# Kernel tuning notes

Hardware: AMD Instinct MI355X
Metric: run time of the kernel (lower is better)

Reference implementation:

```python
import jax, jax.numpy as jnp
import numpy as np

EPS = 1e-15


def _trace(t):
    return jnp.einsum('bii->b', t)


def _ortho_loss(ss, k):
    n = jnp.linalg.norm(ss, axis=(-1, -2), keepdims=True)
    diff = ss / n - jnp.eye(k, dtype=ss.dtype) / np.float32(np.sqrt(k))
    return jnp.mean(jnp.linalg.norm(diff, axis=(-1, -2)))


def _mincut_terms(s, adj):
    out_adj = jnp.einsum('bnk,bnm,bml->bkl', s, adj, s)
    d_flat = adj.sum(-1)  # degrees [B,N]
    num = _trace(out_adj)
    den = _trace(jnp.einsum('bnk,bn,bnl->bkl', s, d_flat, s)) + EPS
    return out_adj, num, den, d_flat


def dense_mincut_rewiring(x, adj, s, mask):
    k = s.shape[-1]  # 2
    m = mask[..., None].astype(x.dtype)
    s = jax.nn.softmax(s, axis=-1) * m
    _, num, den, _ = _mincut_terms(s, adj)
    mincut_loss = -jnp.mean(num / den)
    ortho_loss = _ortho_loss(jnp.einsum('bnk,bnl->bkl', s, s), k)
    # laplacian derivative of spectral gap wrt A_uv: (f_u - f_v)^2, f = soft bipartition
    f = s[..., 0]
    dlam = (f[:, :, None] - f[:, None, :]) ** 2
    return adj * (1.0 - dlam), mincut_loss, ortho_loss


def dense_CT_rewiring(x, adj, s, mask):
    k = s.shape[-1]
    m = mask[..., None].astype(x.dtype)
    s = jax.nn.softmax(s, axis=-1) * m
    d_flat = adj.sum(-1)
    sds = _trace(jnp.einsum('bnk,bn,bnl->bkl', s, d_flat, s))
    sas = _trace(jnp.einsum('bnk,bnm,bml->bkl', s, adj, s))
    den = _trace(jnp.einsum('bnk,bnl->bkl', s, s)) + EPS
    ct_loss = jnp.mean((sds - sas) / den)  # tr(Z^T L Z) / tr(Z^T Z)
    ortho_loss = _ortho_loss(jnp.einsum('bnk,bnl->bkl', s, s), k)
    # pairwise CT distances ||z_u - z_v|| / vol(G), sparsified by A
    sq = (s * s).sum(-1)
    d2 = sq[:, :, None] + sq[:, None, :] - 2.0 * jnp.einsum('bnk,bmk->bnm', s, s)
    ct_dist = jnp.sqrt(jnp.maximum(d2, 0.0) + 1e-12)
    vol = d_flat.sum(-1)
    new_adj = (ct_dist / (vol[:, None, None] + EPS)) * adj
    return new_adj, ct_loss, ortho_loss


def dense_mincut_pool(x, adj, s, mask):
    k = s.shape[-1]
    m = mask[..., None].astype(x.dtype)
    s = jax.nn.softmax(s, axis=-1) * m
    x = x * m
    out = jnp.einsum('bnk,bnf->bkf', s, x)
    out_adj, num, den, _ = _mincut_terms(s, adj)
    mincut_loss = -jnp.mean(num / den)
    ortho_loss = _ortho_loss(jnp.einsum('bnk,bnl->bkl', s, s), k)
    out_adj = out_adj * (1.0 - jnp.eye(k, dtype=adj.dtype))  # zero diagonal
    d = jnp.sqrt(out_adj.sum(-1)) + EPS  # [B,k]
    out_adj = out_adj / d[:, None, :] / d[:, :, None]
    return out, out_adj, mincut_loss, ortho_loss


def _dgc(x, adj, w_rel, b_rel, w_root):
    # DenseGraphConv(aggr='add'): lin_rel(A @ x) + lin_root(x)
    return jnp.matmul(adj, x) @ w_rel + b_rel + x @ w_root


def setup_inputs() -> dict:
    B, N, IN, H, KC, OUT, KMC = 16, 1024, 128, 32, 32, 10, 16
    keys = iter(jax.random.split(jax.random.key(0), 48))

    def lin(fin, fout):
        lim = float(1.0 / np.sqrt(fin))
        return (jax.random.uniform(next(keys), (fin, fout), jnp.float32, -lim, lim),
                jax.random.uniform(next(keys), (fout,), jnp.float32, -lim, lim))

    x = jax.random.normal(next(keys), (B, N, IN), jnp.float32)
    u = jax.random.uniform(next(keys), (B, N, N), jnp.float32)
    a = (u < 0.0156).astype(jnp.float32)  # avg degree ~16
    adj = jnp.maximum(a, jnp.swapaxes(a, 1, 2)) * (1.0 - jnp.eye(N, dtype=jnp.float32))
    mask = jnp.ones((B, N), dtype=bool)
    W1, b1 = lin(IN, H)
    Wrw, brw = lin(H, 2)
    Wg_rel, bg = lin(H, H); Wg_root, _ = lin(H, H)
    Wmcg, bmcg = lin(H, KMC)
    W2g_rel, b2g = lin(H, H); W2g_root, _ = lin(H, H)
    Wct, bct = lin(H, KC)
    Wc_rel, bc = lin(H, H); Wc_root, _ = lin(H, H)
    Wmcc, bmcc = lin(H, KMC)
    Wcat, bcat = lin(2 * H, H)
    W2, b2 = lin(H, H)
    W3, b3 = lin(H, OUT)
    return dict(x=x, adj=adj, mask=mask, W1=W1, b1=b1, Wrw=Wrw, brw=brw,
                Wg_rel=Wg_rel, bg=bg, Wg_root=Wg_root, Wmcg=Wmcg, bmcg=bmcg,
                W2g_rel=W2g_rel, b2g=b2g, W2g_root=W2g_root, Wct=Wct, bct=bct,
                Wc_rel=Wc_rel, bc=bc, Wc_root=Wc_root, Wmcc=Wmcc, bmcc=bmcc,
                Wcat=Wcat, bcat=bcat, W2=W2, b2=b2, W3=W3, b3=b3)


def reference(x, adj, mask, W1, b1, Wrw, brw, Wg_rel, bg, Wg_root, Wmcg, bmcg,
              W2g_rel, b2g, W2g_root, Wct, bct, Wc_rel, bc, Wc_root, Wmcc, bmcc,
              Wcat, bcat, W2, b2, W3, b3):
    x = x @ W1 + b1
    # GAP branch
    adj_gap, mc_rw, ol_rw = dense_mincut_rewiring(x, adj, x @ Wrw + brw, mask)
    x_gap = _dgc(x, adj_gap, Wg_rel, bg, Wg_root)
    x_gap, adj_gap, mc1, ol1 = dense_mincut_pool(x_gap, adj_gap, x_gap @ Wmcg + bmcg, mask)
    x_gap = _dgc(x_gap, adj_gap, W2g_rel, b2g, W2g_root)
    # CT branch
    adj_ct, ct_loss, ol_ct = dense_CT_rewiring(x, adj, x @ Wct + bct, mask)
    x_ct = _dgc(x, adj_ct, Wc_rel, bc, Wc_root)
    x_ct, adj_ct, mc2, ol2 = dense_mincut_pool(x_ct, adj_ct, x_ct @ Wmcc + bmcc, mask)
    x_ct = _dgc(x_ct, adj_ct, W2g_rel, b2g, W2g_root)  # source reuses self.conv2gap here
    h = jax.nn.relu(jnp.concatenate([x_gap, x_ct], axis=2) @ Wcat + bcat).sum(axis=1)
    h = jax.nn.relu(h @ W2 + b2)
    logits = h @ W3 + b3
    main_loss = mc_rw + ct_loss + mc1 + mc2
    ortho_loss = ol_rw + ol_ct + ol1 + ol2
    return (jax.nn.log_softmax(logits, axis=-1), main_loss, ortho_loss)
```

## Files before the change

### kernel.cpp

```cpp
#include <hip/hip_runtime.h>
#include <math.h>

#define BB   16
#define NNODE 1024
#define INF_ 128
#define HH   32
#define KMC  16
#define CAP  128
#define EPS15 1e-15f

typedef float v4f __attribute__((ext_vector_type(4)));

#define OFF_X      0
#define OFF_SRW    524288
#define OFF_SQCT   557056
#define OFF_SCT    573440
#define OFF_D      1097728
#define OFF_NUMRW  1114112
#define OFF_SAS    1130496
#define OFF_DGAP   1146880
#define OFF_DCT    1163264
#define OFF_XGAP   2228224
#define OFF_XCT    2752512
#define OFF_S2G    3276800
#define OFF_S2C    3538944
#define OFF_FROB   4325376
#define OFF_VOL    4325888
#define OFF_OUTG   4326032
#define OFF_OUTC   4334224
#define OFF_G2G    4342416
#define OFF_G2C    4346512
#define OFF_OAG    4350608
#define OFF_OAC    4354704
#define OFF_ENNZ   4358800
#define OFF_EIDX   4375184
#define OFF_EWG    5423760
#define OFF_EWC    7520912
#define OFF_PACK   9618064
#define OFF_BSUM   9683600

__device__ __forceinline__ float wave_sum(float v) {
#pragma unroll
  for (int off = 32; off >= 1; off >>= 1) v += __shfl_xor(v, off, 64);
  return v;
}

__device__ __forceinline__ void wave_sum4(float& a, float& b, float& c, float& d) {
#pragma unroll
  for (int off = 32; off >= 1; off >>= 1) {
    a += __shfl_xor(a, off, 64);
    b += __shfl_xor(b, off, 64);
    c += __shfl_xor(c, off, 64);
    d += __shfl_xor(d, off, 64);
  }
}

__device__ __forceinline__ float blk_sum(float v, float* sred, int tid) {
  v = wave_sum(v);
  __syncthreads();
  if ((tid & 63) == 0) sred[tid >> 6] = v;
  __syncthreads();
  return sred[0] + sred[1] + sred[2] + sred[3];
}

__device__ __forceinline__ void blk_sum5(float* v, float (*sm)[4], int tid) {
  int w = tid >> 6, lane = tid & 63;
#pragma unroll
  for (int i = 0; i < 5; i++) {
#pragma unroll
    for (int off = 32; off >= 1; off >>= 1) v[i] += __shfl_xor(v[i], off, 64);
  }
  if (lane == 0) {
#pragma unroll
    for (int i = 0; i < 5; i++) sm[i][w] = v[i];
  }
  __syncthreads();
#pragma unroll
  for (int i = 0; i < 5; i++) v[i] = sm[i][0] + sm[i][1] + sm[i][2] + sm[i][3];
}

__global__ __launch_bounds__(256) void k_fused0(
    const float* __restrict__ adj, const float* __restrict__ x,
    const float* __restrict__ W1, const float* __restrict__ b1,
    const float* __restrict__ Wrw, const float* __restrict__ brw,
    const float* __restrict__ Wct, const float* __restrict__ bct,
    float* __restrict__ ws)
{
  __shared__ __align__(16) float sW1[INF_*HH];
  __shared__ __align__(16) float sWct[HH*HH];
  __shared__ float sWrw[HH*2];
  __shared__ float sb1[HH], sbct[HH], sbrw[2];
  __shared__ __align__(16) float sx[8*INF_];
  __shared__ float sX[8*HH];
  __shared__ unsigned int s_e32[4][4][CAP/2];
  int tid = threadIdx.x;
  if (blockIdx.x < 1024) {
    int w = tid >> 6, lane = tid & 63;
    int row0 = blockIdx.x * 16 + w * 4;
    v4f v[16];
#pragma unroll
    for (int rr = 0; rr < 4; rr++) {
      const v4f* ar = (const v4f*)(adj + (size_t)(row0 + rr) * NNODE);
#pragma unroll
      for (int it = 0; it < 4; it++)
        v[rr*4 + it] = __builtin_nontemporal_load(&ar[it*64 + lane]);
    }
#pragma unroll
    for (int rr = 0; rr < 4; rr++) {
      int row = row0 + rr;
      int c = 0;
#pragma unroll
      for (int it = 0; it < 4; it++) {
        v4f a4 = v[rr*4 + it];
        c += (a4.x != 0.f) + (a4.y != 0.f) + (a4.z != 0.f) + (a4.w != 0.f);
      }
      int p = c;
#pragma unroll
      for (int off = 1; off < 64; off <<= 1) {
        int t = __shfl_up(p, off, 64);
        if (lane >= off) p += t;
      }
      int excl = p - c;
      int total = __shfl(p, 63, 64);
      unsigned short* es = (unsigned short*)s_e32[w][rr];
      int pos = excl;
#pragma unroll
      for (int it = 0; it < 4; it++) {
        v4f a4 = v[rr*4 + it];
        int m0 = it*256 + lane*4;
        if (a4.x != 0.f) { if (pos < CAP) es[pos] = (unsigned short)(m0+0); pos++; }
        if (a4.y != 0.f) { if (pos < CAP) es[pos] = (unsigned short)(m0+1); pos++; }
        if (a4.z != 0.f) { if (pos < CAP) es[pos] = (unsigned short)(m0+2); pos++; }
        if (a4.w != 0.f) { if (pos < CAP) es[pos] = (unsigned short)(m0+3); pos++; }
      }
      int nnzc = total < CAP ? total : CAP;
      unsigned int* dst = (unsigned int*)((unsigned short*)(ws + OFF_EIDX) + (size_t)row*CAP);
      int n32 = (nnzc + 1) >> 1;
      if (lane < n32) dst[lane] = s_e32[w][rr][lane];
      if (lane == 0) {
        ((int*)(ws + OFF_ENNZ))[row] = nnzc;
        ws[OFF_D + row] = (float)total;
      }
    }
  } else {
    for (int i = tid; i < INF_*HH/4; i += 256)
      ((float4*)sW1)[i] = ((const float4*)W1)[i];
    ((float4*)sWct)[tid] = ((const float4*)Wct)[tid];
    if (tid < HH*2) sWrw[tid] = Wrw[tid];
    if (tid < HH) { sb1[tid] = b1[tid]; sbct[tid] = bct[tid]; }
    if (tid < 2) sbrw[tid] = brw[tid];
    size_t row0 = (size_t)(blockIdx.x - 1024) * 8;
    ((float4*)sx)[tid] = ((const float4*)(x + row0 * INF_))[tid];
    __syncthreads();
    int r = tid >> 5, h = tid & 31;
    float acc = sb1[h];
#pragma unroll 8
    for (int k = 0; k < INF_; k++) acc += sx[r*INF_ + k] * sW1[k*HH + h];
    size_t row = row0 + r;
    ws[OFF_X + row*HH + h] = acc;
    sX[r*HH + h] = acc;
    __syncthreads();
    float sraw = sbct[h];
#pragma unroll
    for (int k = 0; k < HH; k++) sraw += sX[r*HH + k] * sWct[k*HH + h];
    float mx = sraw;
#pragma unroll
    for (int off = 16; off >= 1; off >>= 1) mx = fmaxf(mx, __shfl_xor(mx, off, 32));
    float e = __expf(sraw - mx);
    float sum = e;
#pragma unroll
    for (int off = 16; off >= 1; off >>= 1) sum += __shfl_xor(sum, off, 32);
    float sv = e / sum;
    ws[OFF_SCT + row*HH + h] = sv;
    float sq = sv * sv;
#pragma unroll
    for (int off = 16; off >= 1; off >>= 1) sq += __shfl_xor(sq, off, 32);
    float xv = sX[r*HH + h];
    float t0 = xv * sWrw[h*2 + 0];
    float t1 = xv * sWrw[h*2 + 1];
#pragma unroll
    for (int off = 16; off >= 1; off >>= 1) { t0 += __shfl_xor(t0, off, 32); t1 += __shfl_xor(t1, off, 32); }
    if (h == 0) {
      ws[OFF_SQCT + row] = sq;
      float r0 = t0 + sbrw[0], r1 = t1 + sbrw[1];
      float m2 = fmaxf(r0, r1);
      float e0 = __expf(r0 - m2), e1 = __expf(r1 - m2);
      float inv = 1.0f / (e0 + e1);
      float s0 = e0*inv, s1 = e1*inv;
      ((float2*)(ws + OFF_SRW))[row] = make_float2(s0, s1);
      ((float4*)(ws + OFF_PACK))[row] = make_float4(s0, s1, sq, 0.f);
    }
  }
}

__global__ __launch_bounds__(256) void k_edgefeat(
    const float* __restrict__ Wg_rel, const float* __restrict__ bg, const float* __restrict__ Wg_root,
    const float* __restrict__ Wc_rel, const float* __restrict__ bc, const float* __restrict__ Wc_root,
    const float* __restrict__ Wmcg, const float* __restrict__ bmcg,
    const float* __restrict__ Wmcc, const float* __restrict__ bmcc,
    float* __restrict__ out, float* __restrict__ ws)
{
  __shared__ unsigned short s_m[4][CAP];
  __shared__ float s_wg[4][CAP];
  __shared__ float s_wc[4][CAP];
  __shared__ float sp[8][32];
  __shared__ float sred[4];
  __shared__ __align__(16) float sWgrel[HH*HH], sWgroot[HH*HH], sWcrel[HH*HH], sWcroot[HH*HH];
  __shared__ float sbg[HH], sbc[HH];
  __shared__ float sYg[4*HH], sYc[4*HH], sXr[4*HH], sxg[4*HH], sxc[4*HH];
  int tid = threadIdx.x;
  if (blockIdx.x < 4096) {
    int xcd = blockIdx.x & 7;
    int idx = blockIdx.x >> 3;
    int b = xcd*2 + (idx >> 8);
    int chunk = idx & 255;
    int base4 = b*NNODE + chunk*4;
    ((float4*)sWgrel)[tid]  = ((const float4*)Wg_rel)[tid];
    ((float4*)sWgroot)[tid] = ((const float4*)Wg_root)[tid];
    ((float4*)sWcrel)[tid]  = ((const float4*)Wc_rel)[tid];
    ((float4*)sWcroot)[tid] = ((const float4*)Wc_root)[tid];
    if (tid < HH)  { sbg[tid] = bg[tid]; sbc[tid] = bc[tid]; }
    if (tid < 128) sXr[tid] = ws[OFF_X + (size_t)base4*HH + tid];
    float vp = 0.f;
#pragma unroll
    for (int i = 0; i < 4; i++) vp += ws[OFF_D + (size_t)b*NNODE + tid + i*256];

    const float* X = ws + OFF_X;
    const float2* srw = (const float2*)(ws + OFF_SRW);
    const float* sqct = ws + OFF_SQCT;
    const float* sct = ws + OFF_SCT;
    const float4* pack = (const float4*)(ws + OFF_PACK) + (size_t)b*NNODE;
    int w = tid >> 6, lane = tid & 63;
    int tm = lane & 3;
    int row = base4 + w;
    int nnz = ((const int*)(ws + OFF_ENNZ))[row];
    const unsigned short* eidx = (const unsigned short*)(ws + OFF_EIDX) + (size_t)row*CAP;
    const float4* cn4 = (const float4*)(sct + (size_t)row * HH);
    float4 c0 = cn4[tm*2], c1 = cn4[tm*2 + 1];
    float2 srwn = srw[row];
    float f_n = srwn.x;
    float sq_n = sqct[row];
    float numrw_p = 0.f, sas_p = 0.f, dg_p = 0.f, dc_p = 0.f;
    for (int e = (lane >> 2); e < nnz; e += 16) {
      int m = eidx[e];
      const float4* cm4 = (const float4*)(sct + ((size_t)b*NNODE + m) * HH);
      float4 d0 = cm4[tm*2], d1 = cm4[tm*2 + 1];
      float dot = c0.x*d0.x + c0.y*d0.y + c0.z*d0.z + c0.w*d0.w
                + c1.x*d1.x + c1.y*d1.y + c1.z*d1.z + c1.w*d1.w;
      dot += __shfl_xor(dot, 1, 64);
      dot += __shfl_xor(dot, 2, 64);
      float4 pk = pack[m];
      numrw_p += srwn.x*pk.x + srwn.y*pk.y;
      float df = f_n - pk.x;
      float wg = 1.0f - df*df;
      float d2 = sq_n + pk.z - 2.0f*dot;
      float wc = sqrtf(fmaxf(d2, 0.0f) + 1e-12f);
      sas_p += dot;
      dg_p += wg;
      dc_p += wc;
      if (tm == 0) {
        s_m[w][e] = (unsigned short)m;
        s_wg[w][e] = wg;
        s_wc[w][e] = wc;
        size_t eo = (size_t)row*CAP + e;
        ws[OFF_EWG + eo] = wg;
        ws[OFF_EWC + eo] = wc;
      }
    }
    wave_sum4(numrw_p, sas_p, dg_p, dc_p);
    if (lane == 0) {
      ws[OFF_NUMRW + row] = numrw_p * 0.25f;
      ws[OFF_SAS + row] = sas_p * 0.25f;
      ws[OFF_DGAP + row] = dg_p * 0.25f;
      ws[OFF_DCT + row] = dc_p * 0.25f;
    }
    int eoff = lane >> 4, hp = lane & 15;
    float yg0 = 0.f, yg1 = 0.f, yc0 = 0.f, yc1 = 0.f;
    for (int e = eoff; e < nnz; e += 4) {
      int m = s_m[w][e];
      float wg = s_wg[w][e], wc = s_wc[w][e];
      float2 xv = ((const float2*)(X + ((size_t)b*NNODE + m)*HH))[hp];
      yg0 += wg*xv.x; yg1 += wg*xv.y;
      yc0 += wc*xv.x; yc1 += wc*xv.y;
    }
    yg0 += __shfl_xor(yg0, 16, 64); yg0 += __shfl_xor(yg0, 32, 64);
    yg1 += __shfl_xor(yg1, 16, 64); yg1 += __shfl_xor(yg1, 32, 64);
    yc0 += __shfl_xor(yc0, 16, 64); yc0 += __shfl_xor(yc0, 32, 64);
    yc1 += __shfl_xor(yc1, 16, 64); yc1 += __shfl_xor(yc1, 32, 64);
    if (eoff == 0) {
      sYg[w*HH + 2*hp] = yg0; sYg[w*HH + 2*hp + 1] = yg1;
      sYc[w*HH + 2*hp] = yc0; sYc[w*HH + 2*hp + 1] = yc1;
    }
    float vol = blk_sum(vp, sred, tid);
    float ivol = 1.0f / (vol + EPS15);
    {
      int r = tid >> 6;
      int h = (tid >> 1) & 31;
      int half = tid & 1;
      int kb = half * 16;
      float accg = 0.f, accg2 = 0.f, accc = 0.f, accc2 = 0.f;
#pragma unroll
      for (int kk = 0; kk < 16; kk++) {
        int k = kb + kk;
        float ygv = sYg[r*HH + k], Xv = sXr[r*HH + k], ycv = sYc[r*HH + k];
        accg  += ygv * sWgrel[k*HH + h];
        accg2 += Xv  * sWgroot[k*HH + h];
        accc  += ycv * sWcrel[k*HH + h];
        accc2 += Xv  * sWcroot[k*HH + h];
      }
      accg  += __shfl_xor(accg, 1, 64);
      accg2 += __shfl_xor(accg2, 1, 64);
      accc  += __shfl_xor(accc, 1, 64);
      accc2 += __shfl_xor(accc2, 1, 64);
      if (half == 0) {
        float xgv = sbg[h] + accg + accg2;
        float xcv = sbc[h] + ivol*accc + accc2;
        size_t rw = (size_t)base4 + r;
        ws[OFF_XGAP + rw*HH + h] = xgv;
        ws[OFF_XCT  + rw*HH + h] = xcv;
        sxg[r*HH + h] = xgv;
        sxc[r*HH + h] = xcv;
      }
    }
    __syncthreads();
    if (tid < 128) {
      int r = tid >> 5, h = tid & 31;
      int j = h & 15, halfsel = h >> 4;
      const float* sin_ = halfsel ? sxc : sxg;
      const float* sw = halfsel ? Wmcc : Wmcg;
      float raw = halfsel ? bmcc[j] : bmcg[j];
#pragma unroll
      for (int k = 0; k < HH; k++) raw += sin_[r*HH + k] * sw[k*KMC + j];
      float mx = raw;
#pragma unroll
      for (int off = 8; off >= 1; off >>= 1) mx = fmaxf(mx, __shfl_xor(mx, off, 16));
      float e = __expf(raw - mx);
      float sum = e;
#pragma unroll
      for (int off = 8; off >= 1; off >>= 1) sum += __shfl_xor(sum, off, 16);
      float sv = e / sum;
      size_t rw = (size_t)base4 + r;
      if (halfsel == 0) ws[OFF_S2G + rw*KMC + j] = sv;
      else              ws[OFF_S2C + rw*KMC + j] = sv;
    }
  } else if (blockIdx.x < 4608) {
    int blk = blockIdx.x - 4096;
    int xcd = blk & 7;
    int idx = blk >> 3;
    int b = xcd*2 + (idx >> 5);
    int i = idx & 31;
    const float* sct = ws + OFF_SCT + (size_t)b*NNODE*HH;
    int j = tid & 31, seg = tid >> 5;
    float acc = 0.f;
    for (int n = seg*128; n < seg*128 + 128; n++)
      acc += sct[n*HH + i] * sct[n*HH + j];
    sp[seg][j] = acc;
    __syncthreads();
    if (tid < 32) {
      float g = 0.f;
#pragma unroll
      for (int s = 0; s < 8; s++) g += sp[s][tid];
      float p = g * g;
#pragma unroll
      for (int off = 16; off >= 1; off >>= 1) p += __shfl_xor(p, off, 32);
      if (tid == 0) ws[OFF_FROB + b*32 + i] = p;
    }
  } else {
    int b = blockIdx.x - 4608;
    if (b == 0 && tid < 2) out[160 + tid] = 0.f;
    if (tid < 12) ws[OFF_BSUM + b*12 + tid] = 0.f;
    for (int i = tid; i < 2048; i += 256) ws[OFF_OUTG + b*2048 + i] = 0.f;
    float vp = 0.f;
    for (int n = tid; n < NNODE; n += 256) vp += ws[OFF_D + (size_t)b*NNODE + n];
    float vol = blk_sum(vp, sred, tid);
    if (tid == 0) ws[OFF_VOL + b] = vol;
  }
}

__global__ __launch_bounds__(512) void k_passred(float* __restrict__ ws)
{
  __shared__ float sg[32*16], sc[32*16], stg[32*16], stc[32*16];
  __shared__ float sxg[32*32], sxc[32*32];
  int xcd = blockIdx.x & 7;
  int idx = blockIdx.x >> 3;
  int b = xcd*2 + (idx >> 5);
  int chunk = idx & 31;
  int tid = threadIdx.x;
  size_t n0 = (size_t)b * NNODE + chunk * 32;
  const float* pG  = ws + OFF_S2G  + n0 * KMC;
  const float* pC  = ws + OFF_S2C  + n0 * KMC;
  const float* pXG = ws + OFF_XGAP + n0 * HH;
  const float* pXC = ws + OFF_XCT  + n0 * HH;
  sg[tid] = pG[tid];
  sc[tid] = pC[tid];
  sxg[tid] = pXG[tid]; sxg[tid + 512] = pXG[tid + 512];
  sxc[tid] = pXC[tid]; sxc[tid + 512] = pXC[tid + 512];
  {
    int r = tid >> 4, k = tid & 15;
    size_t row = n0 + r;
    int nnz = ((const int*)(ws + OFF_ENNZ))[row];
    const unsigned short* eidx = (const unsigned short*)(ws + OFF_EIDX) + row * CAP;
    const float* ewg = ws + OFF_EWG + row * CAP;
    const float* ewc = ws + OFF_EWC + row * CAP;
    const float* S2G = ws + OFF_S2G + (size_t)b * NNODE * KMC;
    const float* S2C = ws + OFF_S2C + (size_t)b * NNODE * KMC;
    float ag = 0.f, ac = 0.f;
    int e = 0;
    for (; e + 1 < nnz; e += 2) {
      int m0 = eidx[e], m1 = eidx[e + 1];
      float g0 = ewg[e], g1 = ewg[e + 1];
      float c0 = ewc[e], c1 = ewc[e + 1];
      ag += g0 * S2G[(size_t)m0 * KMC + k] + g1 * S2G[(size_t)m1 * KMC + k];
      ac += c0 * S2C[(size_t)m0 * KMC + k] + c1 * S2C[(size_t)m1 * KMC + k];
    }
    if (e < nnz) {
      int m = eidx[e];
      ag += ewg[e] * S2G[(size_t)m * KMC + k];
      ac += ewc[e] * S2C[(size_t)m * KMC + k];
    }
    stg[r * 16 + k] = ag;
    stc[r * 16 + k] = ac;
  }
  __syncthreads();
  int sub = tid >> 8, t = tid & 255;
  { int k0 = t >> 5, h0 = t & 31;
    float og0 = 0.f, og1 = 0.f, oc0 = 0.f, oc1 = 0.f;
#pragma unroll
    for (int i = 0; i < 16; i++) {
      int r = sub * 16 + i;
      float xgv = sxg[r*32 + h0], xcv = sxc[r*32 + h0];
      og0 += sg[r*16 + k0]     * xgv;
      og1 += sg[r*16 + k0 + 8] * xgv;
      oc0 += sc[r*16 + k0]     * xcv;
      oc1 += sc[r*16 + k0 + 8] * xcv;
    }
    atomicAdd(&ws[OFF_OUTG + b*512 + k0*32 + h0],     og0);
    atomicAdd(&ws[OFF_OUTG + b*512 + (k0+8)*32 + h0], og1);
    atomicAdd(&ws[OFF_OUTC + b*512 + k0*32 + h0],     oc0);
    atomicAdd(&ws[OFF_OUTC + b*512 + (k0+8)*32 + h0], oc1);
  }
  { int kk = t >> 4, l = t & 15;
    float gg = 0.f, gc = 0.f, ag = 0.f, ac = 0.f;
#pragma unroll
    for (int i = 0; i < 16; i++) {
      int r = sub * 16 + i;
      float sgk = sg[r*16 + kk], sck = sc[r*16 + kk];
      gg += sgk * sg [r*16 + l];
      gc += sck * sc [r*16 + l];
      ag += sgk * stg[r*16 + l];
      ac += sck * stc[r*16 + l];
    }
    atomicAdd(&ws[OFF_G2G + b*256 + t], gg);
    atomicAdd(&ws[OFF_G2C + b*256 + t], gc);
    atomicAdd(&ws[OFF_OAG + b*256 + t], ag);
    atomicAdd(&ws[OFF_OAC + b*256 + t], ac);
  }
  if (tid < 32) {
    size_t gn = n0 + tid;
    float ng = 0.f, nc = 0.f;
#pragma unroll
    for (int j = 0; j < KMC; j++) {
      float a = sg[tid*16 + j], c2 = sc[tid*16 + j];
      ng += a*a; nc += c2*c2;
    }
    float dgv = ws[OFF_DGAP + gn];
    float dcv = ws[OFF_DCT + gn];
    float d   = ws[OFF_D + gn];
    float2 s  = ((const float2*)(ws + OFF_SRW))[gn];
    float sq  = ws[OFF_SQCT + gn];
    float nmr = ws[OFF_NUMRW + gn];
    float sasv= ws[OFF_SAS + gn];
    float u0 = dgv*ng, u1 = dcv*nc, u2 = ng, u3 = nc;
    float u4 = d*(s.x*s.x + s.y*s.y), u5 = nmr, u6 = d*sq, u7 = sasv;
    float u8 = sq, u9 = s.x*s.x, u10 = s.x*s.y, u11 = s.y*s.y;
#pragma unroll
    for (int off = 16; off >= 1; off >>= 1) {
      u0 += __shfl_xor(u0, off, 32);  u1 += __shfl_xor(u1, off, 32);
      u2 += __shfl_xor(u2, off, 32);  u3 += __shfl_xor(u3, off, 32);
      u4 += __shfl_xor(u4, off, 32);  u5 += __shfl_xor(u5, off, 32);
      u6 += __shfl_xor(u6, off, 32);  u7 += __shfl_xor(u7, off, 32);
      u8 += __shfl_xor(u8, off, 32);  u9 += __shfl_xor(u9, off, 32);
      u10 += __shfl_xor(u10, off, 32); u11 += __shfl_xor(u11, off, 32);
    }
    if (tid == 0) {
      float* bs = ws + OFF_BSUM + b*12;
      atomicAdd(bs + 0, u0);  atomicAdd(bs + 1, u1);  atomicAdd(bs + 2, u2);
      atomicAdd(bs + 3, u3);  atomicAdd(bs + 4, u4);  atomicAdd(bs + 5, u5);
      atomicAdd(bs + 6, u6);  atomicAdd(bs + 7, u7);  atomicAdd(bs + 8, u8);
      atomicAdd(bs + 9, u9);  atomicAdd(bs + 10, u10); atomicAdd(bs + 11, u11);
    }
  }
}

__global__ __launch_bounds__(256) void k_batch2(
    const float* __restrict__ W2g_rel, const float* __restrict__ b2g, const float* __restrict__ W2g_root,
    const float* __restrict__ Wcat, const float* __restrict__ bcat,
    const float* __restrict__ W2, const float* __restrict__ b2,
    const float* __restrict__ W3, const float* __restrict__ b3,
    float* __restrict__ out, float* __restrict__ ws)
{
  __shared__ float sOAg[256], sOAc[256], sOutg[512], sOutc[512];
  __shared__ float sW2grel[1024], sW2groot[1024], sWcat[2048], sW2l[1024];
  __shared__ float sPg[512], sPc[512], sXg2[512], sXc2[512], sHt[512];
  __shared__ float sHs[32], sH2[32], sLg[16], sScal[2];
  __shared__ float sdkg[16], sdkc[16];
  __shared__ float smm[5][4];
  int b = blockIdx.x, tid = threadIdx.x;
  sOAg[tid] = ws[OFF_OAG + b*256 + tid];
  sOAc[tid] = ws[OFF_OAC + b*256 + tid];
  sOutg[tid]       = ws[OFF_OUTG + b*512 + tid];
  sOutg[tid + 256] = ws[OFF_OUTG + b*512 + tid + 256];
  sOutc[tid]       = ws[OFF_OUTC + b*512 + tid];
  sOutc[tid + 256] = ws[OFF_OUTC + b*512 + tid + 256];
  for (int i = tid; i < 1024; i += 256) { sW2grel[i] = W2g_rel[i]; sW2groot[i] = W2g_root[i]; sW2l[i] = W2[i]; }
  for (int i = tid; i < 2048; i += 256) sWcat[i] = Wcat[i];
  float v[5];
  v[0] = (tid < 32) ? ws[OFF_FROB + b*32 + tid] : 0.f;
  float gv = ws[OFF_G2G + b*256 + tid];
  float cv = ws[OFF_G2C + b*256 + tid];
  v[1] = gv*gv; v[2] = cv*cv;
  __syncthreads();
  v[3] = (tid < 16) ? sOAg[tid*17] : 0.f;
  v[4] = (tid < 16) ? sOAc[tid*17] : 0.f;
  blk_sum5(v, smm, tid);
  float frob2 = v[0], frobg2 = v[1], frobc2 = v[2], num1 = v[3], num2u = v[4];
  float vol = ws[OFF_VOL + b];
  float ivol = 1.0f / (vol + EPS15);
  if (tid == 0) {
    const float* bs = ws + OFF_BSUM + b*12;
    float den1 = bs[0], den2u = bs[1], trg = bs[2], trc = bs[3];
    float denrw = bs[4], num = bs[5], sds = bs[6], sas = bs[7], denct = bs[8];
    float g00 = bs[9], g01 = bs[10], g11 = bs[11];
    float mcrw = -num / (denrw + EPS15);
    float ctb  = (sds - sas) / (denct + EPS15);
    float nrw = sqrtf(g00*g00 + 2.f*g01*g01 + g11*g11);
    float olrw = sqrtf(fmaxf(2.f - 2.f*(g00 + g11)/(nrw*1.41421356237f), 0.f));
    float nct = sqrtf(frob2);
    float olct = sqrtf(fmaxf(2.f - 2.f*denct/(nct*5.65685424949f), 0.f));
    float mc1 = -num1 / (den1 + EPS15);
    float mc2 = -(num2u*ivol) / (den2u*ivol + EPS15);
    float ol1 = sqrtf(fmaxf(2.f - 2.f*trg/(sqrtf(frobg2)*4.f), 0.f));
    float ol2 = sqrtf(fmaxf(2.f - 2.f*trc/(sqrtf(frobc2)*4.f), 0.f));
    atomicAdd(out + 160, (mcrw + ctb + mc1 + mc2) * 0.0625f);
    atomicAdd(out + 161, (olrw + olct + ol1 + ol2) * 0.0625f);
  }
  sOAc[tid] *= ivol;
  __syncthreads();
  if (tid < 16) { sOAg[tid*17] = 0.f; sOAc[tid*17] = 0.f; }
  __syncthreads();
  if (tid < 16) {
    float rg = 0.f, rc = 0.f;
#pragma unroll
    for (int l = 0; l < 16; l++) { rg += sOAg[tid*16 + l]; rc += sOAc[tid*16 + l]; }
    sdkg[tid] = sqrtf(rg) + EPS15;
    sdkc[tid] = sqrtf(rc) + EPS15;
  }
  __syncthreads();
  { int k = tid >> 4, l = tid & 15;
    sOAg[tid] /= (sdkg[k]*sdkg[l]);
    sOAc[tid] /= (sdkc[k]*sdkc[l]); }
  __syncthreads();
  { int k = tid >> 5, h = tid & 31;
    float p0 = 0, p1 = 0, q0 = 0, q1 = 0;
#pragma unroll
    for (int l = 0; l < 16; l++) {
      p0 += sOAg[k*16 + l] * sOutg[l*32 + h];
      p1 += sOAg[(k+8)*16 + l] * sOutg[l*32 + h];
      q0 += sOAc[k*16 + l] * sOutc[l*32 + h];
      q1 += sOAc[(k+8)*16 + l] * sOutc[l*32 + h];
    }
    sPg[k*32 + h] = p0; sPg[(k+8)*32 + h] = p1;
    sPc[k*32 + h] = q0; sPc[(k+8)*32 + h] = q1;
  }
  __syncthreads();
  { int k = tid >> 5, h = tid & 31;
    float bb2 = b2g[h];
    float a0 = bb2, a1 = bb2, c0 = bb2, c1 = bb2;
#pragma unroll
    for (int q = 0; q < 32; q++) {
      float wr = sW2grel[q*32 + h], wo = sW2groot[q*32 + h];
      a0 += sPg[k*32 + q]*wr + sOutg[k*32 + q]*wo;
      a1 += sPg[(k+8)*32 + q]*wr + sOutg[(k+8)*32 + q]*wo;
      c0 += sPc[k*32 + q]*wr + sOutc[k*32 + q]*wo;
      c1 += sPc[(k+8)*32 + q]*wr + sOutc[(k+8)*32 + q]*wo;
    }
    sXg2[k*32 + h] = a0; sXg2[(k+8)*32 + h] = a1;
    sXc2[k*32 + h] = c0; sXc2[(k+8)*32 + h] = c1;
  }
  __syncthreads();
  { int k = tid >> 5, h = tid & 31;
    float bb = bcat[h];
    float t0 = bb, t1 = bb;
#pragma unroll
    for (int q = 0; q < 32; q++) {
      float w1v = sWcat[q*32 + h], w2v = sWcat[(q+32)*32 + h];
      t0 += sXg2[k*32 + q]*w1v + sXc2[k*32 + q]*w2v;
      t1 += sXg2[(k+8)*32 + q]*w1v + sXc2[(k+8)*32 + q]*w2v;
    }
    sHt[k*32 + h] = fmaxf(t0, 0.f);
    sHt[(k+8)*32 + h] = fmaxf(t1, 0.f);
  }
  __syncthreads();
  if (tid < 32) {
    float s = 0.f;
#pragma unroll
    for (int k = 0; k < 16; k++) s += sHt[k*32 + tid];
    sHs[tid] = s;
  }
  __syncthreads();
  if (tid < 32) {
    float a = b2[tid];
#pragma unroll
    for (int q = 0; q < 32; q++) a += sHs[q]*sW2l[q*32 + tid];
    sH2[tid] = fmaxf(a, 0.f);
  }
  __syncthreads();
  if (tid < 10) {
    float a = b3[tid];
#pragma unroll
    for (int q = 0; q < 32; q++) a += sH2[q]*W3[q*10 + tid];
    sLg[tid] = a;
  }
  __syncthreads();
  if (tid == 0) {
    float m = sLg[0];
    for (int o = 1; o < 10; o++) m = fmaxf(m, sLg[o]);
    float se = 0.f;
    for (int o = 0; o < 10; o++) se += __expf(sLg[o] - m);
    sScal[0] = m; sScal[1] = logf(se);
  }
  __syncthreads();
  if (tid < 10) out[b*10 + tid] = sLg[tid] - sScal[0] - sScal[1];
}

extern "C" void kernel_launch(void* const* d_in, const int* in_sizes, int n_in,
                              void* d_out, int out_size, void* d_ws, size_t ws_size,
                              hipStream_t stream)
{
  const float* x       = (const float*)d_in[0];
  const float* adj     = (const float*)d_in[1];
  const float* W1      = (const float*)d_in[3];
  const float* b1      = (const float*)d_in[4];
  const float* Wrw     = (const float*)d_in[5];
  const float* brw     = (const float*)d_in[6];
  const float* Wg_rel  = (const float*)d_in[7];
  const float* bg      = (const float*)d_in[8];
  const float* Wg_root = (const float*)d_in[9];
  const float* Wmcg    = (const float*)d_in[10];
  const float* bmcg    = (const float*)d_in[11];
  const float* W2g_rel = (const float*)d_in[12];
  const float* b2g     = (const float*)d_in[13];
  const float* W2g_root= (const float*)d_in[14];
  const float* Wct     = (const float*)d_in[15];
  const float* bct     = (const float*)d_in[16];
  const float* Wc_rel  = (const float*)d_in[17];
  const float* bc      = (const float*)d_in[18];
  const float* Wc_root = (const float*)d_in[19];
  const float* Wmcc    = (const float*)d_in[20];
  const float* bmcc    = (const float*)d_in[21];
  const float* Wcat    = (const float*)d_in[22];
  const float* bcat    = (const float*)d_in[23];
  const float* W2      = (const float*)d_in[24];
  const float* b2      = (const float*)d_in[25];
  const float* W3      = (const float*)d_in[26];
  const float* b3      = (const float*)d_in[27];
  float* out = (float*)d_out;
  float* ws  = (float*)d_ws;

  k_fused0<<<dim3(3072), dim3(256), 0, stream>>>(adj, x, W1, b1, Wrw, brw, Wct, bct, ws);
  k_edgefeat<<<dim3(4624), dim3(256), 0, stream>>>(Wg_rel, bg, Wg_root, Wc_rel, bc, Wc_root,
                                                   Wmcg, bmcg, Wmcc, bmcc, out, ws);
  k_passred<<<dim3(512), dim3(512), 0, stream>>>(ws);
  k_batch2<<<dim3(16), dim3(256), 0, stream>>>(W2g_rel, b2g, W2g_root, Wcat, bcat,
                                               W2, b2, W3, b3, out, ws);
}
```

Measured before the change: 243.0 us.

## Move CT Gram matrix computation into passred with atomic accumulation

Result: no change. 247.3 us (+1.8%).

```diff
diff --git a/kernel.cpp b/kernel.cpp
--- a/kernel.cpp
+++ b/kernel.cpp
@@ -38,6 +38,7 @@
 #define OFF_EWC    7520912
 #define OFF_PACK   9618064
 #define OFF_BSUM   9683600
+#define OFF_GRAM   9683800
 
 __device__ __forceinline__ float wave_sum(float v) {
 #pragma unroll
@@ -203,15 +204,25 @@
   __shared__ unsigned short s_m[4][CAP];
   __shared__ float s_wg[4][CAP];
   __shared__ float s_wc[4][CAP];
-  __shared__ float sp[8][32];
   __shared__ float sred[4];
   __shared__ __align__(16) float sWgrel[HH*HH], sWgroot[HH*HH], sWcrel[HH*HH], sWcroot[HH*HH];
   __shared__ float sbg[HH], sbc[HH];
   __shared__ float sYg[4*HH], sYc[4*HH], sXr[4*HH], sxg[4*HH], sxc[4*HH];
   int tid = threadIdx.x;
-  if (blockIdx.x < 4096) {
-    int xcd = blockIdx.x & 7;
-    int idx = blockIdx.x >> 3;
+  if (blockIdx.x < 16) {
+    int b = blockIdx.x;
+    if (b == 0 && tid < 2) out[160 + tid] = 0.f;
+    if (tid < 12) ws[OFF_BSUM + b*12 + tid] = 0.f;
+    for (int i = tid; i < 1024; i += 256) ws[OFF_GRAM + b*1024 + i] = 0.f;
+    for (int i = tid; i < 2048; i += 256) ws[OFF_OUTG + b*2048 + i] = 0.f;
+    float vp = 0.f;
+    for (int n = tid; n < NNODE; n += 256) vp += ws[OFF_D + (size_t)b*NNODE + n];
+    float vol = blk_sum(vp, sred, tid);
+    if (tid == 0) ws[OFF_VOL + b] = vol;
+  } else {
+    int eb = blockIdx.x - 16;
+    int xcd = eb & 7;
+    int idx = eb >> 3;
     int b = xcd*2 + (idx >> 8);
     int chunk = idx & 255;
     int base4 = b*NNODE + chunk*4;
@@ -343,37 +354,6 @@
       if (halfsel == 0) ws[OFF_S2G + rw*KMC + j] = sv;
       else              ws[OFF_S2C + rw*KMC + j] = sv;
     }
-  } else if (blockIdx.x < 4608) {
-    int blk = blockIdx.x - 4096;
-    int xcd = blk & 7;
-    int idx = blk >> 3;
-    int b = xcd*2 + (idx >> 5);
-    int i = idx & 31;
-    const float* sct = ws + OFF_SCT + (size_t)b*NNODE*HH;
-    int j = tid & 31, seg = tid >> 5;
-    float acc = 0.f;
-    for (int n = seg*128; n < seg*128 + 128; n++)
-      acc += sct[n*HH + i] * sct[n*HH + j];
-    sp[seg][j] = acc;
-    __syncthreads();
-    if (tid < 32) {
-      float g = 0.f;
-#pragma unroll
-      for (int s = 0; s < 8; s++) g += sp[s][tid];
-      float p = g * g;
-#pragma unroll
-      for (int off = 16; off >= 1; off >>= 1) p += __shfl_xor(p, off, 32);
-      if (tid == 0) ws[OFF_FROB + b*32 + i] = p;
-    }
-  } else {
-    int b = blockIdx.x - 4608;
-    if (b == 0 && tid < 2) out[160 + tid] = 0.f;
-    if (tid < 12) ws[OFF_BSUM + b*12 + tid] = 0.f;
-    for (int i = tid; i < 2048; i += 256) ws[OFF_OUTG + b*2048 + i] = 0.f;
-    float vp = 0.f;
-    for (int n = tid; n < NNODE; n += 256) vp += ws[OFF_D + (size_t)b*NNODE + n];
-    float vol = blk_sum(vp, sred, tid);
-    if (tid == 0) ws[OFF_VOL + b] = vol;
   }
 }
 
@@ -381,6 +361,7 @@
 {
   __shared__ float sg[32*16], sc[32*16], stg[32*16], stc[32*16];
   __shared__ float sxg[32*32], sxc[32*32];
+  __shared__ float ssct[32*32];
   int xcd = blockIdx.x & 7;
   int idx = blockIdx.x >> 3;
   int b = xcd*2 + (idx >> 5);
@@ -391,10 +372,12 @@
   const float* pC  = ws + OFF_S2C  + n0 * KMC;
   const float* pXG = ws + OFF_XGAP + n0 * HH;
   const float* pXC = ws + OFF_XCT  + n0 * HH;
+  const float* pS  = ws + OFF_SCT  + n0 * HH;
   sg[tid] = pG[tid];
   sc[tid] = pC[tid];
   sxg[tid] = pXG[tid]; sxg[tid + 512] = pXG[tid + 512];
   sxc[tid] = pXC[tid]; sxc[tid + 512] = pXC[tid + 512];
+  ssct[tid] = pS[tid]; ssct[tid + 512] = pS[tid + 512];
   {
     int r = tid >> 4, k = tid & 15;
     size_t row = n0 + r;
@@ -422,6 +405,18 @@
     stc[r * 16 + k] = ac;
   }
   __syncthreads();
+  {
+    int i0 = tid >> 5, j0 = tid & 31;
+    float g0 = 0.f, g1 = 0.f;
+#pragma unroll 8
+    for (int r = 0; r < 32; r++) {
+      float sj = ssct[r*32 + j0];
+      g0 += ssct[r*32 + i0] * sj;
+      g1 += ssct[r*32 + i0 + 16] * sj;
+    }
+    atomicAdd(&ws[OFF_GRAM + b*1024 + i0*32 + j0], g0);
+    atomicAdd(&ws[OFF_GRAM + b*1024 + (i0+16)*32 + j0], g1);
+  }
   int sub = tid >> 8, t = tid & 255;
   { int k0 = t >> 5, h0 = t & 31;
     float og0 = 0.f, og1 = 0.f, oc0 = 0.f, oc1 = 0.f;
@@ -515,7 +510,9 @@
   for (int i = tid; i < 1024; i += 256) { sW2grel[i] = W2g_rel[i]; sW2groot[i] = W2g_root[i]; sW2l[i] = W2[i]; }
   for (int i = tid; i < 2048; i += 256) sWcat[i] = Wcat[i];
   float v[5];
-  v[0] = (tid < 32) ? ws[OFF_FROB + b*32 + tid] : 0.f;
+  { const float* G = ws + OFF_GRAM + b*1024;
+    float a0 = G[tid], a1 = G[tid + 256], a2 = G[tid + 512], a3 = G[tid + 768];
+    v[0] = a0*a0 + a1*a1 + a2*a2 + a3*a3; }
   float gv = ws[OFF_G2G + b*256 + tid];
   float cv = ws[OFF_G2C + b*256 + tid];
   v[1] = gv*gv; v[2] = cv*cv;
@@ -668,7 +665,7 @@
   float* ws  = (float*)d_ws;
 
   k_fused0<<<dim3(3072), dim3(256), 0, stream>>>(adj, x, W1, b1, Wrw, brw, Wct, bct, ws);
-  k_edgefeat<<<dim3(4624), dim3(256), 0, stream>>>(Wg_rel, bg, Wg_root, Wc_rel, bc, Wc_root,
+  k_edgefeat<<<dim3(4112), dim3(256), 0, stream>>>(Wg_rel, bg, Wg_root, Wc_rel, bc, Wc_root,
                                                    Wmcg, bmcg, Wmcc, bmcc, out, ws);
   k_passred<<<dim3(512), dim3(512), 0, stream>>>(ws);
   k_batch2<<<dim3(16), dim3(256), 0, stream>>>(W2g_rel, b2g, W2g_root, Wcat, bcat,
```
